# Kernel tuning notes

Hardware: AMD Instinct MI355X
Metric: run time of the kernel (lower is better)

The kernel has to match this reference:

```python
import jax, jax.numpy as jnp
import numpy as np

DT = 0.01  # ODE integration step (init kwarg dt)
B, S, I, H, O = 64, 4096, 128, 256, 128


def setup_inputs() -> dict:
    key = jax.random.key(0)
    k0, k1, k2, k3 = jax.random.split(key, 4)
    x = jax.random.normal(k0, (B, S, I), jnp.float32)
    # LTC cell parameters: Linear(in+hidden -> hidden), per-neuron tau and A
    W = jax.random.normal(k1, (I + H, H), jnp.float32) / np.sqrt(I + H)
    b = jnp.zeros((H,), jnp.float32)
    tau = jnp.ones((H,), jnp.float32)
    A = jax.random.normal(k2, (H,), jnp.float32)
    # output Linear(hidden -> out)
    Wo = jax.random.normal(k3, (H, O), jnp.float32) / np.sqrt(H)
    bo = jnp.zeros((O,), jnp.float32)
    return {"x": x, "W": W, "b": b, "tau": tau, "A": A, "Wo": Wo, "bo": bo}


def reference(x, W, b, tau, A, Wo, bo):
    # x: [B, S, I]; recurrence over S with LTC fused semi-implicit ODE step.
    h0 = jnp.zeros((x.shape[0], W.shape[1]), x.dtype)

    def step(h, x_t):
        # f = tanh(Linear([x_t, h]))
        f = jnp.tanh(jnp.concatenate([x_t, h], axis=-1) @ W + b)  # [B, H]
        # fused LTC solver: h' = (h + dt*f*A) / (1 + dt*(1/tau + f))
        h_new = (h + DT * f * A) / (1.0 + DT * (1.0 / tau + f))
        return h_new, None

    h_final, _ = jax.lax.scan(step, h0, jnp.swapaxes(x, 0, 1))  # scan over time
    return h_final @ Wo + bo  # [B, O]
```

## Files before the change

kernel.cpp:

```cpp
#include <hip/hip_runtime.h>
#include <math.h>

#define DT    0.01f
#define B_    64
#define S_    4096
#define I_    128
#define H_    256
#define O_    128

typedef _Float16 f16x8 __attribute__((ext_vector_type(8)));
typedef float    f32x4 __attribute__((ext_vector_type(4)));

#define RPB 64

__global__ __launch_bounds__(256, 2) void xproj_kernel(
    const float* __restrict__ x, const float* __restrict__ W,
    const float* __restrict__ bias, float* __restrict__ xp)
{
  __shared__ __align__(16) float xs[RPB][I_];
  const int j = threadIdx.x;

  float w[I_];
#pragma unroll
  for (int k = 0; k < I_; ++k) w[k] = W[k * H_ + j];
  const float bj = bias[j];

  const size_t row0 = (size_t)blockIdx.x * RPB;

  const float4* src4 = (const float4*)(x + row0 * I_);
  float4* xs4 = (float4*)&xs[0][0];
#pragma unroll
  for (int i = 0; i < (RPB * I_ / 4) / 256; ++i)
    xs4[j + i * 256] = src4[j + i * 256];
  __syncthreads();

  for (int r = 0; r < RPB; r += 4) {
    float a0 = bj, a1 = bj, a2 = bj, a3 = bj;
    const float4* r0 = (const float4*)xs[r + 0];
    const float4* r1 = (const float4*)xs[r + 1];
    const float4* r2 = (const float4*)xs[r + 2];
    const float4* r3 = (const float4*)xs[r + 3];
#pragma unroll
    for (int k4 = 0; k4 < I_ / 4; ++k4) {
      float4 v0 = r0[k4], v1 = r1[k4], v2 = r2[k4], v3 = r3[k4];
      a0 = fmaf(v0.x, w[4*k4+0], a0); a0 = fmaf(v0.y, w[4*k4+1], a0);
      a0 = fmaf(v0.z, w[4*k4+2], a0); a0 = fmaf(v0.w, w[4*k4+3], a0);
      a1 = fmaf(v1.x, w[4*k4+0], a1); a1 = fmaf(v1.y, w[4*k4+1], a1);
      a1 = fmaf(v1.z, w[4*k4+2], a1); a1 = fmaf(v1.w, w[4*k4+3], a1);
      a2 = fmaf(v2.x, w[4*k4+0], a2); a2 = fmaf(v2.y, w[4*k4+1], a2);
      a2 = fmaf(v2.z, w[4*k4+2], a2); a2 = fmaf(v2.w, w[4*k4+3], a2);
      a3 = fmaf(v3.x, w[4*k4+0], a3); a3 = fmaf(v3.y, w[4*k4+1], a3);
      a3 = fmaf(v3.z, w[4*k4+2], a3); a3 = fmaf(v3.w, w[4*k4+3], a3);
    }
    xp[(row0 + r + 0) * H_ + j] = a0;
    xp[(row0 + r + 1) * H_ + j] = a1;
    xp[(row0 + r + 2) * H_ + j] = a2;
    xp[(row0 + r + 3) * H_ + j] = a3;
  }
}

__global__ __launch_bounds__(512, 2) void ltc_main(
    const float* __restrict__ xp, const float* __restrict__ W,
    const float* __restrict__ tau, const float* __restrict__ A,
    const float* __restrict__ Wo, const float* __restrict__ bo,
    float* __restrict__ out)
{
  const int b  = blockIdx.x;
  const int t  = threadIdx.x;
  const int wv = t >> 6;
  const int l  = t & 63;
  const int g  = l >> 4;
  const int c  = l & 15;
  const int s  = l >> 5;
  const int o  = wv * 32 + s * 16 + c;

  f16x8 bw[2][8];
#pragma unroll
  for (int sg = 0; sg < 2; ++sg)
#pragma unroll
    for (int kt = 0; kt < 8; ++kt)
#pragma unroll
      for (int j = 0; j < 8; ++j)
        bw[sg][kt][j] =
            (_Float16)W[(I_ + kt * 32 + g * 8 + j) * H_ + (wv * 32 + sg * 16 + c)];

  __shared__ __align__(16) _Float16 hs[2][H_];
  __shared__ float hfin[H_];

  const float Aj   = A[o];
  const float itau = 1.0f / tau[o];
  const float dtA  = DT * Aj;
  const float base = 1.0f + DT * itau;

  const float* xprow = xp + (size_t)b * S_ * H_ + o;

  float h    = 0.0f;
  float xpre = xprow[0];
  if (t < H_) hs[0][t] = (_Float16)0.0f;
  __syncthreads();

#define LTC_BODY(RB, WB, STEP)                                               \
  {                                                                          \
    const _Float16* hb = &hs[RB][g * 8];                                     \
    f16x8 a[8];                                                              \
    _Pragma("unroll")                                                        \
    for (int kt = 0; kt < 8; ++kt) a[kt] = *(const f16x8*)(hb + kt * 32);    \
    const int snext = ((STEP) + 1 < S_) ? (STEP) + 1 : (STEP);               \
    const float xnext = xprow[(size_t)snext * H_];                           \
    f32x4 ac00 = {xpre, xpre, xpre, xpre};                                   \
    f32x4 ac01 = {0.f, 0.f, 0.f, 0.f};                                      \
    f32x4 ac10 = {xpre, xpre, xpre, xpre};                                   \
    f32x4 ac11 = {0.f, 0.f, 0.f, 0.f};                                      \
    __builtin_amdgcn_s_setprio(1);                                           \
    _Pragma("unroll")                                                        \
    for (int kt = 0; kt < 4; ++kt) {                                         \
      ac00 = __builtin_amdgcn_mfma_f32_16x16x32_f16(a[kt], bw[0][kt], ac00,  \
                                                    0, 0, 0);                \
      ac10 = __builtin_amdgcn_mfma_f32_16x16x32_f16(a[kt], bw[1][kt], ac10,  \
                                                    0, 0, 0);                \
      ac01 = __builtin_amdgcn_mfma_f32_16x16x32_f16(a[kt + 4], bw[0][kt + 4],\
                                                    ac01, 0, 0, 0);          \
      ac11 = __builtin_amdgcn_mfma_f32_16x16x32_f16(a[kt + 4], bw[1][kt + 4],\
                                                    ac11, 0, 0, 0);          \
    }                                                                        \
    __builtin_amdgcn_s_setprio(0);                                           \
    const float z0 = ac00[0] + ac01[0];                                      \
    const float z1 = ac10[0] + ac11[0];                                      \
    float z = (l & 32) ? z1 : z0;                                            \
    z = fminf(15.0f, fmaxf(-15.0f, z));                                      \
    const float E = __expf(2.0f * z);                                        \
    const float f = (E - 1.0f) * __builtin_amdgcn_rcpf(E + 1.0f);            \
    h = fmaf(dtA, f, h) * __builtin_amdgcn_rcpf(fmaf(DT, f, base));          \
    if (!(l & 16)) hs[WB][o] = (_Float16)h;                                  \
    xpre = xnext;                                                            \
    __syncthreads();                                                         \
  }

  for (int st = 0; st < S_; st += 2) {
    LTC_BODY(0, 1, st)
    LTC_BODY(1, 0, st + 1)
  }
#undef LTC_BODY

  if (!(l & 16)) hfin[o] = h;
  __syncthreads();

  if (t < O_) {
    float accO = bo[t];
#pragma unroll 8
    for (int hh = 0; hh < H_; ++hh)
      accO = fmaf(hfin[hh], Wo[hh * O_ + t], accO);
    out[b * O_ + t] = accO;
  }
}

__global__ __launch_bounds__(1024) void ltc_inline(
    const float* __restrict__ x, const float* __restrict__ W,
    const float* __restrict__ bias, const float* __restrict__ tau,
    const float* __restrict__ A, const float* __restrict__ Wo,
    const float* __restrict__ bo, float* __restrict__ out)
{
  const int b = blockIdx.x;
  const int t = threadIdx.x;
  const int j = t & (H_ - 1);
  const int c = t >> 8;

  float wh[64], wx[32];
#pragma unroll
  for (int kk = 0; kk < 64; ++kk)
    wh[kk] = W[(I_ + c * 64 + kk) * H_ + j];
#pragma unroll
  for (int kk = 0; kk < 32; ++kk)
    wx[kk] = W[(c * 32 + kk) * H_ + j];

  __shared__ __align__(16) float hsf[H_];
  __shared__ __align__(16) float xsf[I_];
  __shared__ float ps[3][H_];

  float Aj = 0.f, itau = 0.f, bj = 0.f;
  if (c == 0) {
    Aj = A[j];
    itau = 1.0f / tau[j];
    bj = bias[j];
    hsf[j] = 0.0f;
  }
  const float4* xrow4 = (const float4*)(x + (size_t)b * S_ * I_);
  if (t < 32) ((float4*)xsf)[t] = xrow4[t];
  __syncthreads();

  for (int step = 0; step < S_; ++step) {
    float4 xnext4 = make_float4(0.f, 0.f, 0.f, 0.f);
    if (t < 32) {
      const int snext = (step + 1 < S_) ? step + 1 : step;
      xnext4 = xrow4[snext * 32 + t];
    }

    float acc = 0.0f;
#pragma unroll
    for (int kk = 0; kk < 64; kk += 4) {
      float4 h4 = *(const float4*)&hsf[c * 64 + kk];
      acc = fmaf(h4.x, wh[kk + 0], acc);
      acc = fmaf(h4.y, wh[kk + 1], acc);
      acc = fmaf(h4.z, wh[kk + 2], acc);
      acc = fmaf(h4.w, wh[kk + 3], acc);
    }
#pragma unroll
    for (int kk = 0; kk < 32; kk += 4) {
      float4 x4 = *(const float4*)&xsf[c * 32 + kk];
      acc = fmaf(x4.x, wx[kk + 0], acc);
      acc = fmaf(x4.y, wx[kk + 1], acc);
      acc = fmaf(x4.z, wx[kk + 2], acc);
      acc = fmaf(x4.w, wx[kk + 3], acc);
    }

    if (c) ps[c - 1][j] = acc;
    __syncthreads();

    if (t < 32) ((float4*)xsf)[t] = xnext4;
    if (c == 0) {
      const float z = acc + ps[0][j] + ps[1][j] + ps[2][j] + bj;
      const float f = tanhf(z);
      const float hj = hsf[j];
      hsf[j] = (hj + DT * f * Aj) / (1.0f + DT * (itau + f));
    }
    __syncthreads();
  }

  if (t < O_) {
    float acc = bo[t];
#pragma unroll 8
    for (int h = 0; h < H_; ++h)
      acc = fmaf(hsf[h], Wo[h * O_ + t], acc);
    out[b * O_ + t] = acc;
  }
}

extern "C" void kernel_launch(void* const* d_in, const int* in_sizes, int n_in,
                              void* d_out, int out_size, void* d_ws, size_t ws_size,
                              hipStream_t stream) {
  const float* x   = (const float*)d_in[0];
  const float* W   = (const float*)d_in[1];
  const float* b   = (const float*)d_in[2];
  const float* tau = (const float*)d_in[3];
  const float* A   = (const float*)d_in[4];
  const float* Wo  = (const float*)d_in[5];
  const float* bo  = (const float*)d_in[6];
  float* out = (float*)d_out;

  const size_t XP_BYTES = (size_t)B_ * S_ * H_ * sizeof(float);

  if (ws_size >= XP_BYTES) {
    float* xp = (float*)d_ws;
    hipLaunchKernelGGL(xproj_kernel, dim3((B_ * S_) / RPB), dim3(256), 0, stream,
                       x, W, b, xp);
    hipLaunchKernelGGL(ltc_main, dim3(B_), dim3(512), 0, stream,
                       xp, W, tau, A, Wo, bo, out);
  } else {
    hipLaunchKernelGGL(ltc_inline, dim3(B_), dim3(1024), 0, stream,
                       x, W, b, tau, A, Wo, bo, out);
  }
}
```

Measured before the change: 1.805 ms.

## Split recurrent matvec between MFMA and fdot2, stage xproj chunks in LDS

```diff
diff --git a/kernel.cpp b/kernel.cpp
--- a/kernel.cpp
+++ b/kernel.cpp
@@ -8,8 +8,23 @@
 #define H_    256
 #define O_    128
 
-typedef _Float16 f16x8 __attribute__((ext_vector_type(8)));
-typedef float    f32x4 __attribute__((ext_vector_type(4)));
+typedef _Float16 f16x8  __attribute__((ext_vector_type(8)));
+typedef _Float16 half2v __attribute__((ext_vector_type(2)));
+typedef float    f32x4  __attribute__((ext_vector_type(4)));
+
+#if defined(__has_builtin)
+#if __has_builtin(__builtin_amdgcn_fdot2)
+#define FDOT2(a, b, c) __builtin_amdgcn_fdot2((a), (b), (c), false)
+#endif
+#endif
+#ifndef FDOT2
+#define FDOT2(a, b, c) \
+  fmaf((float)(a).x, (float)(b).x, fmaf((float)(a).y, (float)(b).y, (c)))
+#endif
+
+static __device__ __forceinline__ half2v mkh2(_Float16 a, _Float16 b) {
+  half2v r; r.x = a; r.y = b; return r;
+}
 
 #define RPB 64
 
@@ -70,77 +85,125 @@
   const int wv = t >> 6;
   const int l  = t & 63;
   const int g  = l >> 4;
+  const int gg = g & 1;
   const int c  = l & 15;
   const int s  = l >> 5;
   const int o  = wv * 32 + s * 16 + c;
 
-  f16x8 bw[2][8];
+  f16x8 bw[2][4];
 #pragma unroll
   for (int sg = 0; sg < 2; ++sg)
 #pragma unroll
-    for (int kt = 0; kt < 8; ++kt)
+    for (int kt = 0; kt < 4; ++kt)
 #pragma unroll
       for (int j = 0; j < 8; ++j)
         bw[sg][kt][j] =
             (_Float16)W[(I_ + kt * 32 + g * 8 + j) * H_ + (wv * 32 + sg * 16 + c)];
 
+  half2v wd[32];
+#pragma unroll
+  for (int i = 0; i < 32; ++i) {
+    const int k = I_ + 128 + gg * 64 + 2 * i;
+    wd[i].x = (_Float16)W[k * H_ + o];
+    wd[i].y = (_Float16)W[(k + 1) * H_ + o];
+  }
+
   __shared__ __align__(16) _Float16 hs[2][H_];
   __shared__ float hfin[H_];
+  __shared__ __align__(16) float xs[2][32][H_];
 
   const float Aj   = A[o];
   const float itau = 1.0f / tau[o];
   const float dtA  = DT * Aj;
   const float base = 1.0f + DT * itau;
 
-  const float* xprow = xp + (size_t)b * S_ * H_ + o;
-
-  float h    = 0.0f;
-  float xpre = xprow[0];
+  const float* xpb = xp + (size_t)b * S_ * H_;
+
+  float h = 0.0f;
   if (t < H_) hs[0][t] = (_Float16)0.0f;
+
+  {
+    const float4* s4 = (const float4*)xpb;
+    float4 q0 = s4[t], q1 = s4[t + 512], q2 = s4[t + 1024], q3 = s4[t + 1536];
+    float4* d4 = (float4*)&xs[0][0][0];
+    d4[t] = q0; d4[t + 512] = q1; d4[t + 1024] = q2; d4[t + 1536] = q3;
+  }
   __syncthreads();
 
-#define LTC_BODY(RB, WB, STEP)                                               \
+#define DOT8(HV, W0, W1, W2, W3)                                             \
+  dv0 = FDOT2(mkh2(HV[0], HV[1]), W0, dv0);                                  \
+  dv1 = FDOT2(mkh2(HV[2], HV[3]), W1, dv1);                                  \
+  dv0 = FDOT2(mkh2(HV[4], HV[5]), W2, dv0);                                  \
+  dv1 = FDOT2(mkh2(HV[6], HV[7]), W3, dv1);
+
+#define LTC_BODY(RB, WB, XROW)                                               \
   {                                                                          \
     const _Float16* hb = &hs[RB][g * 8];                                     \
-    f16x8 a[8];                                                              \
-    _Pragma("unroll")                                                        \
-    for (int kt = 0; kt < 8; ++kt) a[kt] = *(const f16x8*)(hb + kt * 32);    \
-    const int snext = ((STEP) + 1 < S_) ? (STEP) + 1 : (STEP);               \
-    const float xnext = xprow[(size_t)snext * H_];                           \
+    f16x8 a0_ = *(const f16x8*)(hb);                                         \
+    f16x8 a1_ = *(const f16x8*)(hb + 32);                                    \
+    f16x8 a2_ = *(const f16x8*)(hb + 64);                                    \
+    f16x8 a3_ = *(const f16x8*)(hb + 96);                                    \
+    const f16x8* h2p = (const f16x8*)&hs[RB][128 + gg * 64];                 \
+    f16x8 hv0 = h2p[0], hv1 = h2p[1], hv2 = h2p[2], hv3 = h2p[3];            \
+    f16x8 hv4 = h2p[4], hv5 = h2p[5], hv6 = h2p[6], hv7 = h2p[7];            \
+    const float xpre = (XROW)[o];                                            \
     f32x4 ac00 = {xpre, xpre, xpre, xpre};                                   \
-    f32x4 ac01 = {0.f, 0.f, 0.f, 0.f};                                      \
+    f32x4 ac01 = {0.f, 0.f, 0.f, 0.f};                                       \
     f32x4 ac10 = {xpre, xpre, xpre, xpre};                                   \
-    f32x4 ac11 = {0.f, 0.f, 0.f, 0.f};                                      \
-    __builtin_amdgcn_s_setprio(1);                                           \
-    _Pragma("unroll")                                                        \
-    for (int kt = 0; kt < 4; ++kt) {                                         \
-      ac00 = __builtin_amdgcn_mfma_f32_16x16x32_f16(a[kt], bw[0][kt], ac00,  \
-                                                    0, 0, 0);                \
-      ac10 = __builtin_amdgcn_mfma_f32_16x16x32_f16(a[kt], bw[1][kt], ac10,  \
-                                                    0, 0, 0);                \
-      ac01 = __builtin_amdgcn_mfma_f32_16x16x32_f16(a[kt + 4], bw[0][kt + 4],\
-                                                    ac01, 0, 0, 0);          \
-      ac11 = __builtin_amdgcn_mfma_f32_16x16x32_f16(a[kt + 4], bw[1][kt + 4],\
-                                                    ac11, 0, 0, 0);          \
-    }                                                                        \
-    __builtin_amdgcn_s_setprio(0);                                           \
+    f32x4 ac11 = {0.f, 0.f, 0.f, 0.f};                                       \
+    ac00 = __builtin_amdgcn_mfma_f32_16x16x32_f16(a0_, bw[0][0], ac00, 0,0,0);\
+    ac10 = __builtin_amdgcn_mfma_f32_16x16x32_f16(a0_, bw[1][0], ac10, 0,0,0);\
+    ac01 = __builtin_amdgcn_mfma_f32_16x16x32_f16(a1_, bw[0][1], ac01, 0,0,0);\
+    ac11 = __builtin_amdgcn_mfma_f32_16x16x32_f16(a1_, bw[1][1], ac11, 0,0,0);\
+    ac00 = __builtin_amdgcn_mfma_f32_16x16x32_f16(a2_, bw[0][2], ac00, 0,0,0);\
+    ac10 = __builtin_amdgcn_mfma_f32_16x16x32_f16(a2_, bw[1][2], ac10, 0,0,0);\
+    ac01 = __builtin_amdgcn_mfma_f32_16x16x32_f16(a3_, bw[0][3], ac01, 0,0,0);\
+    ac11 = __builtin_amdgcn_mfma_f32_16x16x32_f16(a3_, bw[1][3], ac11, 0,0,0);\
+    float dv0 = 0.f, dv1 = 0.f;                                              \
+    DOT8(hv0, wd[0],  wd[1],  wd[2],  wd[3])                                 \
+    DOT8(hv1, wd[4],  wd[5],  wd[6],  wd[7])                                 \
+    DOT8(hv2, wd[8],  wd[9],  wd[10], wd[11])                                \
+    DOT8(hv3, wd[12], wd[13], wd[14], wd[15])                                \
+    DOT8(hv4, wd[16], wd[17], wd[18], wd[19])                                \
+    DOT8(hv5, wd[20], wd[21], wd[22], wd[23])                                \
+    DOT8(hv6, wd[24], wd[25], wd[26], wd[27])                                \
+    DOT8(hv7, wd[28], wd[29], wd[30], wd[31])                                \
+    float zv = dv0 + dv1;                                                    \
+    zv += __int_as_float(                                                    \
+        __builtin_amdgcn_ds_swizzle(__float_as_int(zv), 0x401F));            \
     const float z0 = ac00[0] + ac01[0];                                      \
     const float z1 = ac10[0] + ac11[0];                                      \
-    float z = (l & 32) ? z1 : z0;                                            \
+    float z = ((l & 32) ? z1 : z0) + zv;                                     \
     z = fminf(15.0f, fmaxf(-15.0f, z));                                      \
     const float E = __expf(2.0f * z);                                        \
     const float f = (E - 1.0f) * __builtin_amdgcn_rcpf(E + 1.0f);            \
     h = fmaf(dtA, f, h) * __builtin_amdgcn_rcpf(fmaf(DT, f, base));          \
     if (!(l & 16)) hs[WB][o] = (_Float16)h;                                  \
-    xpre = xnext;                                                            \
     __syncthreads();                                                         \
   }
 
-  for (int st = 0; st < S_; st += 2) {
-    LTC_BODY(0, 1, st)
-    LTC_BODY(1, 0, st + 1)
+  const int NCH = S_ / 32;
+  for (int ch = 0; ch < NCH; ++ch) {
+    float4 p0, p1, p2, p3;
+    const bool pf = (ch + 1 < NCH);
+    if (pf) {
+      const float4* s4 = (const float4*)(xpb + (size_t)(ch + 1) * 32 * H_);
+      p0 = s4[t]; p1 = s4[t + 512]; p2 = s4[t + 1024]; p3 = s4[t + 1536];
+    }
+    const float* xc = &xs[ch & 1][0][0];
+    for (int i = 0; i < 30; i += 2) {
+      LTC_BODY(0, 1, xc + i * H_)
+      LTC_BODY(1, 0, xc + (i + 1) * H_)
+    }
+    LTC_BODY(0, 1, xc + 30 * H_)
+    if (pf) {
+      float4* d4 = (float4*)&xs[(ch + 1) & 1][0][0];
+      d4[t] = p0; d4[t + 512] = p1; d4[t + 1024] = p2; d4[t + 1536] = p3;
+    }
+    LTC_BODY(1, 0, xc + 31 * H_)
   }
 #undef LTC_BODY
+#undef DOT8
 
   if (!(l & 16)) hfin[o] = h;
   __syncthreads();
```

New measurement: 2.388 ms. +32.3%, slower.
